# Performance work log

Hardware: AMD Instinct MI355X
Metric: run time of the kernel (lower is better)

## Reference

```python
import jax, jax.numpy as jnp
import numpy as np

B, S, D_MODEL, H = 4, 2048, 1024, 16
DEPTH = D_MODEL // H  # 64


def setup_inputs() -> dict:
    key = jax.random.key(0)
    ks = jax.random.split(key, 12)
    inp = {
        "v": jax.random.normal(ks[0], (B, S, D_MODEL), jnp.float32),
        "k": jax.random.normal(ks[1], (B, S, D_MODEL), jnp.float32),
        "q": jax.random.normal(ks[2], (B, S, D_MODEL), jnp.float32),
        "mask": jnp.zeros((B, 1, 1, S), jnp.int32),  # unused by the layer
        # Dense(d_model) params (glorot-ish scale)
        "wq": jax.random.normal(ks[3], (D_MODEL, D_MODEL), jnp.float32) / np.sqrt(D_MODEL),
        "bq": jnp.zeros((D_MODEL,), jnp.float32),
        "wk": jax.random.normal(ks[4], (D_MODEL, D_MODEL), jnp.float32) / np.sqrt(D_MODEL),
        "bk": jnp.zeros((D_MODEL,), jnp.float32),
        "wv": jax.random.normal(ks[5], (D_MODEL, D_MODEL), jnp.float32) / np.sqrt(D_MODEL),
        "bv": jnp.zeros((D_MODEL,), jnp.float32),
        # global attention weights: [max_seq_len, 1], stddev=0.1
        "gqw": 0.1 * jax.random.normal(ks[6], (S, 1), jnp.float32),
        "gkw": 0.1 * jax.random.normal(ks[7], (S, 1), jnp.float32),
        "wo": jax.random.normal(ks[8], (D_MODEL, D_MODEL), jnp.float32) / np.sqrt(D_MODEL),
        "bo": jnp.zeros((D_MODEL,), jnp.float32),
    }
    return inp


def _split_heads(x):
    # [B, S, D] -> [B, H, S, depth]
    Bc = x.shape[0]
    return x.reshape(Bc, -1, H, DEPTH).transpose(0, 2, 1, 3)


def reference(v, k, q, mask, wq, bq, wk, bk, wv, bv, gqw, gkw, wo, bo):
    # QKV projections
    qh = _split_heads(q @ wq + bq)  # [B, H, S, depth]
    kh = _split_heads(k @ wk + bk)
    vh = _split_heads(v @ wv + bv)
    # Fastformer additive attention: mul -> seq-sum -> mul -> seq-sum -> mul -> add
    qh = qh * gqw                          # gqw [S,1] broadcasts over [B,H,S,depth]
    gq = jnp.sum(qh, axis=2, keepdims=True)  # global query [B,H,1,depth]
    kh = kh * gq * gkw
    gk = jnp.sum(kh, axis=2, keepdims=True)  # global key [B,H,1,depth]
    out = vh * gk + qh                       # [B,H,S,depth]
    # merge heads and output projection
    out = out.transpose(0, 2, 1, 3).reshape(out.shape[0], -1, D_MODEL)
    return out @ wo + bo
```

## Files before the change

### kernel.cpp

```cpp
#include <hip/hip_runtime.h>

#define DM 1024
#define BATCH 4
#define SEQ 2048
#define M_TOT (BATCH*SEQ)

typedef unsigned short ushort_t;
typedef __bf16 bf16x8 __attribute__((ext_vector_type(8)));
typedef float f32x4 __attribute__((ext_vector_type(4)));
typedef unsigned short u16x8 __attribute__((ext_vector_type(8)));

__device__ __forceinline__ ushort_t f2bf(float f) {
  unsigned u = __builtin_bit_cast(unsigned, f);
  u = (u + 0x7fffu + ((u >> 16) & 1u)) >> 16;
  return (ushort_t)u;
}
__device__ __forceinline__ float bf2f(ushort_t h) {
  unsigned u = ((unsigned)h) << 16;
  return __builtin_bit_cast(float, u);
}

#define GLL(gp, lp)                                                            \
  __builtin_amdgcn_global_load_lds(                                            \
      (const __attribute__((address_space(1))) unsigned int*)(const void*)(gp),\
      (__attribute__((address_space(3))) unsigned int*)(void*)(lp), 16, 0, 0)

__global__ void k_reduce(const float* __restrict__ q, const float* __restrict__ k,
                         const float* __restrict__ v,
                         const float* __restrict__ gqw, const float* __restrict__ gkw,
                         float* __restrict__ qr, float* __restrict__ kr,
                         float* __restrict__ G,
                         ushort_t* __restrict__ qb, ushort_t* __restrict__ vb) {
  const int b = blockIdx.x, dch = blockIdx.y, sch = blockIdx.z;
  const int d = dch * 256 + threadIdx.x;
  const int s0 = sch * (SEQ / 16);
  const size_t base = ((size_t)b * SEQ + s0) * DM + d;
  const float* qp = q + base;
  const float* kp = k + base;
  const float* vp = v + base;
  float aq = 0.f, ak = 0.f;
  for (int i = 0; i < SEQ / 16; ++i) {
    const float qv = qp[(size_t)i * DM];
    aq += gqw[s0 + i] * qv;
    ak += gkw[s0 + i] * kp[(size_t)i * DM];
    qb[base + (size_t)i * DM] = f2bf(qv);
    vb[base + (size_t)i * DM] = f2bf(vp[(size_t)i * DM]);
  }
  atomicAdd(&qr[b * DM + d], aq);
  atomicAdd(&kr[b * DM + d], ak);
  if (b == 0 && dch == 0 && threadIdx.x < SEQ / 16) {
    atomicAdd(&G[0], gqw[s0 + threadIdx.x]);
    atomicAdd(&G[1], gkw[s0 + threadIdx.x]);
  }
}

__global__ void k_gpart(const float* __restrict__ wq, const float* __restrict__ wk,
                        const float* __restrict__ qr, const float* __restrict__ kr,
                        float* __restrict__ qacc, float* __restrict__ kacc) {
  const int d = blockIdx.x * 256 + threadIdx.x;
  const int k0 = blockIdx.y * 32;
  __shared__ float sq[4][32], sk[4][32];
  if (threadIdx.x < 128) {
    const int b = threadIdx.x >> 5, kk = threadIdx.x & 31;
    sq[b][kk] = qr[b * DM + k0 + kk];
    sk[b][kk] = kr[b * DM + k0 + kk];
  }
  __syncthreads();
  float aq[4] = {0.f, 0.f, 0.f, 0.f}, ak[4] = {0.f, 0.f, 0.f, 0.f};
#pragma unroll 8
  for (int kk = 0; kk < 32; ++kk) {
    const float wqv = wq[(size_t)(k0 + kk) * DM + d];
    const float wkv = wk[(size_t)(k0 + kk) * DM + d];
#pragma unroll
    for (int b = 0; b < 4; ++b) {
      aq[b] += sq[b][kk] * wqv;
      ak[b] += sk[b][kk] * wkv;
    }
  }
#pragma unroll
  for (int b = 0; b < 4; ++b) {
    atomicAdd(&qacc[b * DM + d], aq[b]);
    atomicAdd(&kacc[b * DM + d], ak[b]);
  }
}

__global__ void k_gfin(const float* __restrict__ qacc, const float* __restrict__ kacc,
                       const float* __restrict__ bq, const float* __restrict__ bk,
                       const float* __restrict__ G, float* __restrict__ gk) {
  const int i = blockIdx.x * 256 + threadIdx.x;
  const int d = i & (DM - 1);
  const float gqv = qacc[i] + bq[d] * G[0];
  const float gkr = kacc[i] + bk[d] * G[1];
  gk[i] = gqv * gkr;
}

__global__ void k_trans(const float* __restrict__ w0, const float* __restrict__ w1,
                        const float* __restrict__ w2,
                        ushort_t* __restrict__ t0, ushort_t* __restrict__ t1,
                        ushort_t* __restrict__ t2) {
  __shared__ float ls[32][33];
  const float* W = blockIdx.z == 0 ? w0 : (blockIdx.z == 1 ? w1 : w2);
  ushort_t* T = blockIdx.z == 0 ? t0 : (blockIdx.z == 1 ? t1 : t2);
  const int bi = blockIdx.x, bj = blockIdx.y;
#pragma unroll
  for (int p = 0; p < 4; ++p) {
    int e = threadIdx.x + p * 256;
    int r = e >> 5, c = e & 31;
    ls[r][c] = W[(size_t)(bi * 32 + r) * DM + bj * 32 + c];
  }
  __syncthreads();
#pragma unroll
  for (int p = 0; p < 4; ++p) {
    int e = threadIdx.x + p * 256;
    int r = e >> 5, c = e & 31;
    T[(size_t)(bj * 32 + r) * DM + bi * 32 + c] = f2bf(ls[c][r]);
  }
}

__global__ void k_mid(const ushort_t* __restrict__ Vp, const ushort_t* __restrict__ Qs,
                      const float* __restrict__ gk, ushort_t* __restrict__ mid) {
  const size_t i = (size_t)blockIdx.x * 256 + threadIdx.x;
  const int col8 = (int)(i & 127) * 8;
  const int b = (int)(i >> 18);
  u16x8 vv = *(const u16x8*)(Vp + i * 8);
  u16x8 qq = *(const u16x8*)(Qs + i * 8);
  const float4 g0 = *(const float4*)(gk + b * DM + col8);
  const float4 g1 = *(const float4*)(gk + b * DM + col8 + 4);
  float g[8] = {g0.x, g0.y, g0.z, g0.w, g1.x, g1.y, g1.z, g1.w};
  u16x8 o;
#pragma unroll
  for (int j = 0; j < 8; ++j) o[j] = f2bf(bf2f(vv[j]) * g[j] + bf2f(qq[j]));
  *(u16x8*)(mid + i * 8) = o;
}

template <int MODE>
__global__ void k_gemm_db(const ushort_t* __restrict__ A0, const ushort_t* __restrict__ B0,
                          const float* __restrict__ bias0,
                          const ushort_t* __restrict__ A1, const ushort_t* __restrict__ B1,
                          const float* __restrict__ bias1,
                          const float* __restrict__ rs,
                          void* __restrict__ Out0V, void* __restrict__ Out1V) {
  __shared__ __align__(16) ushort_t lsA[3][128 * 32];
  __shared__ __align__(16) ushort_t lsB[3][128 * 32];
  const int z = (MODE == 0) ? blockIdx.z : 0;
  const ushort_t* A  = z ? A1 : A0;
  const ushort_t* Bt = z ? B1 : B0;
  const float* bias  = z ? bias1 : bias0;

  const int tid = threadIdx.x;
  const int w = tid >> 6, lane = tid & 63;
  const int m0 = blockIdx.x * 128, n0 = blockIdx.y * 128;
  const int wr = w >> 1, wc = w & 1;

  const int c0 = w * 2, c1 = c0 + 1;
  const int e0 = c0 * 64 + lane, e1 = c1 * 64 + lane;
  const ushort_t* gA0 = A + (size_t)(m0 + (e0 >> 2)) * DM + (e0 & 3) * 8;
  const ushort_t* gA1 = A + (size_t)(m0 + (e1 >> 2)) * DM + (e1 & 3) * 8;
  const ushort_t* gB0 = Bt + (size_t)(n0 + (e0 >> 2)) * DM + (e0 & 3) * 8;
  const ushort_t* gB1 = Bt + (size_t)(n0 + (e1 >> 2)) * DM + (e1 & 3) * 8;

  int aoff[4], boff[4];
#pragma unroll
  for (int i = 0; i < 4; ++i) {
    aoff[i] = (wr * 64 + i * 16 + (lane & 15)) * 32 + (lane >> 4) * 8;
    boff[i] = (wc * 64 + i * 16 + (lane & 15)) * 32 + (lane >> 4) * 8;
  }

  f32x4 acc[4][4];
#pragma unroll
  for (int i = 0; i < 4; ++i)
#pragma unroll
    for (int j = 0; j < 4; ++j) acc[i][j] = (f32x4){0.f, 0.f, 0.f, 0.f};

  auto STAGE = [&](int buf) {
    GLL(gA0, &lsA[buf][c0 * 512]);
    GLL(gA1, &lsA[buf][c1 * 512]);
    GLL(gB0, &lsB[buf][c0 * 512]);
    GLL(gB1, &lsB[buf][c1 * 512]);
    gA0 += 32; gA1 += 32; gB0 += 32; gB1 += 32;
  };

  STAGE(0);
  STAGE(1);
  int cur = 0, nxt = 2;
#pragma unroll 1
  for (int t = 0; t < 32; ++t) {
    if (t < 31) { asm volatile("s_waitcnt vmcnt(4)" ::: "memory"); }
    else        { asm volatile("s_waitcnt vmcnt(0)" ::: "memory"); }
    __builtin_amdgcn_s_barrier();
    if (t + 2 < 32) {
      STAGE(nxt);
      nxt = (nxt == 2) ? 0 : nxt + 1;
    }
    bf16x8 av[4], bv[4];
#pragma unroll
    for (int i = 0; i < 4; ++i) av[i] = *(const bf16x8*)(&lsA[cur][aoff[i]]);
#pragma unroll
    for (int j = 0; j < 4; ++j) bv[j] = *(const bf16x8*)(&lsB[cur][boff[j]]);
#pragma unroll
    for (int i = 0; i < 4; ++i)
#pragma unroll
      for (int j = 0; j < 4; ++j)
        acc[i][j] = __builtin_amdgcn_mfma_f32_16x16x32_bf16(av[i], bv[j], acc[i][j], 0, 0, 0);
    cur = (cur == 2) ? 0 : cur + 1;
  }

  const int lr = (lane >> 4) * 4, lc = lane & 15;
  const int rbase = m0 + wr * 64, cbase = n0 + wc * 64;
  if constexpr (MODE == 0) {
    if (z == 0) {
      ushort_t* Out = (ushort_t*)Out0V;
#pragma unroll
      for (int j = 0; j < 4; ++j) {
        const int col = cbase + j * 16 + lc;
        const float bs = bias[col];
#pragma unroll
        for (int i = 0; i < 4; ++i)
#pragma unroll
          for (int t = 0; t < 4; ++t) {
            const int row = rbase + i * 16 + lr + t;
            Out[(size_t)row * DM + col] = f2bf((acc[i][j][t] + bs) * rs[row & (SEQ - 1)]);
          }
      }
    } else {
      ushort_t* Out = (ushort_t*)Out1V;
#pragma unroll
      for (int j = 0; j < 4; ++j) {
        const int col = cbase + j * 16 + lc;
        const float bs = bias[col];
#pragma unroll
        for (int i = 0; i < 4; ++i)
#pragma unroll
          for (int t = 0; t < 4; ++t) {
            const int row = rbase + i * 16 + lr + t;
            Out[(size_t)row * DM + col] = f2bf(acc[i][j][t] + bs);
          }
      }
    }
  } else {
    float* Out = (float*)Out0V;
#pragma unroll
    for (int j = 0; j < 4; ++j) {
      const int col = cbase + j * 16 + lc;
      const float bs = bias[col];
#pragma unroll
      for (int i = 0; i < 4; ++i)
#pragma unroll
        for (int t = 0; t < 4; ++t) {
          const int row = rbase + i * 16 + lr + t;
          Out[(size_t)row * DM + col] = acc[i][j][t] + bs;
        }
    }
  }
}

extern "C" void kernel_launch(void* const* d_in, const int* in_sizes, int n_in,
                              void* d_out, int out_size, void* d_ws, size_t ws_size,
                              hipStream_t stream) {
  const float* v   = (const float*)d_in[0];
  const float* k   = (const float*)d_in[1];
  const float* q   = (const float*)d_in[2];
  const float* wq  = (const float*)d_in[4];
  const float* bq  = (const float*)d_in[5];
  const float* wk  = (const float*)d_in[6];
  const float* bk  = (const float*)d_in[7];
  const float* wv  = (const float*)d_in[8];
  const float* bv  = (const float*)d_in[9];
  const float* gqw = (const float*)d_in[10];
  const float* gkw = (const float*)d_in[11];
  const float* wo  = (const float*)d_in[12];
  const float* bo  = (const float*)d_in[13];
  float* out = (float*)d_out;
  float* wsf = (float*)d_ws;

  float* qr   = wsf + 0;
  float* kr   = wsf + 4096;
  float* qacc = wsf + 8192;
  float* kacc = wsf + 12288;
  float* G    = wsf + 16384;
  float* gk   = wsf + 16896;
  ushort_t* qb  = (ushort_t*)((char*)d_ws + (1 << 17));
  ushort_t* vb  = qb + (size_t)M_TOT * DM;
  ushort_t* QsB = vb + (size_t)M_TOT * DM;
  ushort_t* wqT = QsB + (size_t)M_TOT * DM;
  ushort_t* wvT = wqT + (size_t)DM * DM;
  ushort_t* woT = wvT + (size_t)DM * DM;
  ushort_t* midB = qb;
  ushort_t* VpB  = (ushort_t*)out;

  hipMemsetAsync(d_ws, 0, (16384 + 2) * sizeof(float), stream);

  k_reduce<<<dim3(BATCH, DM / 256, 16), 256, 0, stream>>>(q, k, v, gqw, gkw, qr, kr, G, qb, vb);

  k_gpart<<<dim3(DM / 256, DM / 32), 256, 0, stream>>>(wq, wk, qr, kr, qacc, kacc);
  k_gfin<<<(BATCH * DM) / 256, 256, 0, stream>>>(qacc, kacc, bq, bk, G, gk);

  k_trans<<<dim3(32, 32, 3), 256, 0, stream>>>(wq, wv, wo, wqT, wvT, woT);

  k_gemm_db<0><<<dim3(M_TOT / 128, DM / 128, 2), 256, 0, stream>>>(
      qb, wqT, bq, vb, wvT, bv, gqw, QsB, VpB);

  k_mid<<<(M_TOT * (DM / 8)) / 256, 256, 0, stream>>>(VpB, QsB, gk, midB);

  k_gemm_db<1><<<dim3(M_TOT / 128, DM / 128), 256, 0, stream>>>(
      midB, woT, bo, nullptr, nullptr, nullptr, nullptr, out, nullptr);
}
```

Baseline: 143.3 us.

## Fold output projection into Q/V weights and fuse both GEMMs into one

Uses associativity to precompute Wq·Wo and per-batch Wv·diag(gk)·Wo with small 1024^3 GEMMs. The big path then becomes a single K=2048 GEMM over concatenated [gqw·q | v] activations. This removes the separate projection GEMM, the elementwise mid kernel and the bf16 intermediate round-trips. Bias terms are folded into per-column epilogue vectors. The cost is five small weight GEMMs per call and an extra bf16 rounding of the combined weights, which may change accuracy.

```diff
diff --git a/kernel.cpp b/kernel.cpp
--- a/kernel.cpp
+++ b/kernel.cpp
@@ -40,10 +40,11 @@
   const float* vp = v + base;
   float aq = 0.f, ak = 0.f;
   for (int i = 0; i < SEQ / 16; ++i) {
+    const float w = gqw[s0 + i];
     const float qv = qp[(size_t)i * DM];
-    aq += gqw[s0 + i] * qv;
+    aq += w * qv;
     ak += gkw[s0 + i] * kp[(size_t)i * DM];
-    qb[base + (size_t)i * DM] = f2bf(qv);
+    qb[base + (size_t)i * DM] = f2bf(w * qv);
     vb[base + (size_t)i * DM] = f2bf(vp[(size_t)i * DM]);
   }
   atomicAdd(&qr[b * DM + d], aq);
@@ -94,13 +95,18 @@
   gk[i] = gqv * gkr;
 }
 
-__global__ void k_trans(const float* __restrict__ w0, const float* __restrict__ w1,
-                        const float* __restrict__ w2,
-                        ushort_t* __restrict__ t0, ushort_t* __restrict__ t1,
-                        ushort_t* __restrict__ t2) {
+__global__ void k_conv(const float* __restrict__ x, ushort_t* __restrict__ y) {
+  size_t i = (size_t)blockIdx.x * 256 + threadIdx.x;
+  const float4* p = (const float4*)x + i * 2;
+  float4 a = p[0], b = p[1];
+  u16x8 o;
+  o[0] = f2bf(a.x); o[1] = f2bf(a.y); o[2] = f2bf(a.z); o[3] = f2bf(a.w);
+  o[4] = f2bf(b.x); o[5] = f2bf(b.y); o[6] = f2bf(b.z); o[7] = f2bf(b.w);
+  *(u16x8*)(y + i * 8) = o;
+}
+
+__global__ void k_trans(const float* __restrict__ W, ushort_t* __restrict__ T) {
   __shared__ float ls[32][33];
-  const float* W = blockIdx.z == 0 ? w0 : (blockIdx.z == 1 ? w1 : w2);
-  ushort_t* T = blockIdx.z == 0 ? t0 : (blockIdx.z == 1 ? t1 : t2);
   const int bi = blockIdx.x, bj = blockIdx.y;
 #pragma unroll
   for (int p = 0; p < 4; ++p) {
@@ -117,41 +123,54 @@
   }
 }
 
-__global__ void k_mid(const ushort_t* __restrict__ Vp, const ushort_t* __restrict__ Qs,
-                      const float* __restrict__ gk, ushort_t* __restrict__ mid) {
+__global__ void k_wog(const ushort_t* __restrict__ woT, const float* __restrict__ gk,
+                      ushort_t* __restrict__ wogT) {
   const size_t i = (size_t)blockIdx.x * 256 + threadIdx.x;
-  const int col8 = (int)(i & 127) * 8;
-  const int b = (int)(i >> 18);
-  u16x8 vv = *(const u16x8*)(Vp + i * 8);
-  u16x8 qq = *(const u16x8*)(Qs + i * 8);
-  const float4 g0 = *(const float4*)(gk + b * DM + col8);
-  const float4 g1 = *(const float4*)(gk + b * DM + col8 + 4);
+  const size_t c = i * 8;
+  const int j0 = (int)(c & (DM - 1));
+  const int b = (int)(c >> 20);
+  u16x8 wv = *(const u16x8*)(woT + (c & ((1u << 20) - 1)));
+  const float4 g0 = *(const float4*)(gk + b * DM + j0);
+  const float4 g1 = *(const float4*)(gk + b * DM + j0 + 4);
   float g[8] = {g0.x, g0.y, g0.z, g0.w, g1.x, g1.y, g1.z, g1.w};
   u16x8 o;
 #pragma unroll
-  for (int j = 0; j < 8; ++j) o[j] = f2bf(bf2f(vv[j]) * g[j] + bf2f(qq[j]));
-  *(u16x8*)(mid + i * 8) = o;
-}
-
-template <int MODE>
-__global__ void k_gemm_db(const ushort_t* __restrict__ A0, const ushort_t* __restrict__ B0,
-                          const float* __restrict__ bias0,
-                          const ushort_t* __restrict__ A1, const ushort_t* __restrict__ B1,
-                          const float* __restrict__ bias1,
-                          const float* __restrict__ rs,
-                          void* __restrict__ Out0V, void* __restrict__ Out1V) {
+  for (int j = 0; j < 8; ++j) o[j] = f2bf(bf2f(wv[j]) * g[j]);
+  *(u16x8*)(wogT + i * 8) = o;
+}
+
+__global__ void k_bias(const float* __restrict__ wo, const float* __restrict__ bq,
+                       const float* __restrict__ bv, const float* __restrict__ gk,
+                       float* __restrict__ qbias, float* __restrict__ vbias) {
+  const int n = blockIdx.x * 256 + threadIdx.x;
+  const int k0 = blockIdx.y * 32;
+  float aq = 0.f, av[4] = {0.f, 0.f, 0.f, 0.f};
+  for (int kk = 0; kk < 32; ++kk) {
+    const float w = wo[(size_t)(k0 + kk) * DM + n];
+    aq += bq[k0 + kk] * w;
+    const float bw = bv[k0 + kk] * w;
+#pragma unroll
+    for (int b = 0; b < 4; ++b) av[b] += bw * gk[b * DM + k0 + kk];
+  }
+  atomicAdd(&qbias[n], aq);
+#pragma unroll
+  for (int b = 0; b < 4; ++b) atomicAdd(&vbias[b * DM + n], av[b]);
+}
+
+__global__ void k_small(const ushort_t* __restrict__ woT, const ushort_t* __restrict__ wogT,
+                        const ushort_t* __restrict__ wqB, const ushort_t* __restrict__ wvB,
+                        ushort_t* __restrict__ WqoT, ushort_t* __restrict__ WvbT) {
   __shared__ __align__(16) ushort_t lsA[3][128 * 32];
   __shared__ __align__(16) ushort_t lsB[3][128 * 32];
-  const int z = (MODE == 0) ? blockIdx.z : 0;
-  const ushort_t* A  = z ? A1 : A0;
-  const ushort_t* Bt = z ? B1 : B0;
-  const float* bias  = z ? bias1 : bias0;
+  const int z = blockIdx.z;
+  const ushort_t* A  = z == 0 ? woT : wogT + (size_t)(z - 1) * (DM * DM);
+  const ushort_t* Bt = z == 0 ? wqB : wvB;
+  ushort_t* Out      = z == 0 ? WqoT : WvbT + (size_t)(z - 1) * (DM * DM);
 
   const int tid = threadIdx.x;
   const int w = tid >> 6, lane = tid & 63;
   const int m0 = blockIdx.x * 128, n0 = blockIdx.y * 128;
   const int wr = w >> 1, wc = w & 1;
-
   const int c0 = w * 2, c1 = c0 + 1;
   const int e0 = c0 * 64 + lane, e1 = c1 * 64 + lane;
   const ushort_t* gA0 = A + (size_t)(m0 + (e0 >> 2)) * DM + (e0 & 3) * 8;
@@ -172,16 +191,16 @@
 #pragma unroll
     for (int j = 0; j < 4; ++j) acc[i][j] = (f32x4){0.f, 0.f, 0.f, 0.f};
 
-  auto STAGE = [&](int buf) {
-    GLL(gA0, &lsA[buf][c0 * 512]);
-    GLL(gA1, &lsA[buf][c1 * 512]);
-    GLL(gB0, &lsB[buf][c0 * 512]);
-    GLL(gB1, &lsB[buf][c1 * 512]);
-    gA0 += 32; gA1 += 32; gB0 += 32; gB1 += 32;
+  auto STAGE = [&](int tt, int buf) {
+    const int o = tt * 32;
+    GLL(gA0 + o, &lsA[buf][c0 * 512]);
+    GLL(gA1 + o, &lsA[buf][c1 * 512]);
+    GLL(gB0 + o, &lsB[buf][c0 * 512]);
+    GLL(gB1 + o, &lsB[buf][c1 * 512]);
   };
 
-  STAGE(0);
-  STAGE(1);
+  STAGE(0, 0);
+  STAGE(1, 1);
   int cur = 0, nxt = 2;
 #pragma unroll 1
   for (int t = 0; t < 32; ++t) {
@@ -189,7 +208,7 @@
     else        { asm volatile("s_waitcnt vmcnt(0)" ::: "memory"); }
     __builtin_amdgcn_s_barrier();
     if (t + 2 < 32) {
-      STAGE(nxt);
+      STAGE(t + 2, nxt);
       nxt = (nxt == 2) ? 0 : nxt + 1;
     }
     bf16x8 av[4], bv[4];
@@ -207,50 +226,113 @@
 
   const int lr = (lane >> 4) * 4, lc = lane & 15;
   const int rbase = m0 + wr * 64, cbase = n0 + wc * 64;
-  if constexpr (MODE == 0) {
-    if (z == 0) {
-      ushort_t* Out = (ushort_t*)Out0V;
-#pragma unroll
-      for (int j = 0; j < 4; ++j) {
-        const int col = cbase + j * 16 + lc;
-        const float bs = bias[col];
-#pragma unroll
-        for (int i = 0; i < 4; ++i)
-#pragma unroll
-          for (int t = 0; t < 4; ++t) {
-            const int row = rbase + i * 16 + lr + t;
-            Out[(size_t)row * DM + col] = f2bf((acc[i][j][t] + bs) * rs[row & (SEQ - 1)]);
-          }
+#pragma unroll
+  for (int j = 0; j < 4; ++j) {
+    const int col = cbase + j * 16 + lc;
+#pragma unroll
+    for (int i = 0; i < 4; ++i)
+#pragma unroll
+      for (int t = 0; t < 4; ++t) {
+        const int row = rbase + i * 16 + lr + t;
+        Out[(size_t)row * DM + col] = f2bf(acc[i][j][t]);
       }
+  }
+}
+
+__global__ void k_big(const ushort_t* __restrict__ qb, const ushort_t* __restrict__ vb,
+                      const ushort_t* __restrict__ WqoT, const ushort_t* __restrict__ WvbT,
+                      const float* __restrict__ gqw, const float* __restrict__ qbias,
+                      const float* __restrict__ vbias, const float* __restrict__ bo,
+                      float* __restrict__ Out) {
+  __shared__ __align__(16) ushort_t lsA[3][128 * 32];
+  __shared__ __align__(16) ushort_t lsB[3][128 * 32];
+  const int tid = threadIdx.x;
+  const int w = tid >> 6, lane = tid & 63;
+  const int m0 = blockIdx.x * 128, n0 = blockIdx.y * 128;
+  const int b = m0 >> 11;
+  const int wr = w >> 1, wc = w & 1;
+  const int c0 = w * 2, c1 = c0 + 1;
+  const int e0 = c0 * 64 + lane, e1 = c1 * 64 + lane;
+  const size_t offA0 = (size_t)(m0 + (e0 >> 2)) * DM + (e0 & 3) * 8;
+  const size_t offA1 = (size_t)(m0 + (e1 >> 2)) * DM + (e1 & 3) * 8;
+  const size_t offB0 = (size_t)(n0 + (e0 >> 2)) * DM + (e0 & 3) * 8;
+  const size_t offB1 = (size_t)(n0 + (e1 >> 2)) * DM + (e1 & 3) * 8;
+  const ushort_t* gAq0 = qb + offA0;
+  const ushort_t* gAq1 = qb + offA1;
+  const ushort_t* gAv0 = vb + offA0;
+  const ushort_t* gAv1 = vb + offA1;
+  const ushort_t* gBq0 = WqoT + offB0;
+  const ushort_t* gBq1 = WqoT + offB1;
+  const ushort_t* gBv0 = WvbT + (size_t)b * (DM * DM) + offB0;
+  const ushort_t* gBv1 = WvbT + (size_t)b * (DM * DM) + offB1;
+
+  int aoff[4], boff[4];
+#pragma unroll
+  for (int i = 0; i < 4; ++i) {
+    aoff[i] = (wr * 64 + i * 16 + (lane & 15)) * 32 + (lane >> 4) * 8;
+    boff[i] = (wc * 64 + i * 16 + (lane & 15)) * 32 + (lane >> 4) * 8;
+  }
+
+  f32x4 acc[4][4];
+#pragma unroll
+  for (int i = 0; i < 4; ++i)
+#pragma unroll
+    for (int j = 0; j < 4; ++j) acc[i][j] = (f32x4){0.f, 0.f, 0.f, 0.f};
+
+  auto STAGE = [&](int tt, int buf) {
+    const ushort_t *a0, *a1, *b0, *b1;
+    if (tt < 32) {
+      const int o = tt * 32;
+      a0 = gAq0 + o; a1 = gAq1 + o; b0 = gBq0 + o; b1 = gBq1 + o;
     } else {
-      ushort_t* Out = (ushort_t*)Out1V;
-#pragma unroll
-      for (int j = 0; j < 4; ++j) {
-        const int col = cbase + j * 16 + lc;
-        const float bs = bias[col];
-#pragma unroll
-        for (int i = 0; i < 4; ++i)
-#pragma unroll
-          for (int t = 0; t < 4; ++t) {
-            const int row = rbase + i * 16 + lr + t;
-            Out[(size_t)row * DM + col] = f2bf(acc[i][j][t] + bs);
-          }
+      const int o = (tt - 32) * 32;
+      a0 = gAv0 + o; a1 = gAv1 + o; b0 = gBv0 + o; b1 = gBv1 + o;
+    }
+    GLL(a0, &lsA[buf][c0 * 512]);
+    GLL(a1, &lsA[buf][c1 * 512]);
+    GLL(b0, &lsB[buf][c0 * 512]);
+    GLL(b1, &lsB[buf][c1 * 512]);
+  };
+
+  STAGE(0, 0);
+  STAGE(1, 1);
+  int cur = 0, nxt = 2;
+#pragma unroll 1
+  for (int t = 0; t < 64; ++t) {
+    if (t < 63) { asm volatile("s_waitcnt vmcnt(4)" ::: "memory"); }
+    else        { asm volatile("s_waitcnt vmcnt(0)" ::: "memory"); }
+    __builtin_amdgcn_s_barrier();
+    if (t + 2 < 64) {
+      STAGE(t + 2, nxt);
+      nxt = (nxt == 2) ? 0 : nxt + 1;
+    }
+    bf16x8 av[4], bv[4];
+#pragma unroll
+    for (int i = 0; i < 4; ++i) av[i] = *(const bf16x8*)(&lsA[cur][aoff[i]]);
+#pragma unroll
+    for (int j = 0; j < 4; ++j) bv[j] = *(const bf16x8*)(&lsB[cur][boff[j]]);
+#pragma unroll
+    for (int i = 0; i < 4; ++i)
+#pragma unroll
+      for (int j = 0; j < 4; ++j)
+        acc[i][j] = __builtin_amdgcn_mfma_f32_16x16x32_bf16(av[i], bv[j], acc[i][j], 0, 0, 0);
+    cur = (cur == 2) ? 0 : cur + 1;
+  }
+
+  const int lr = (lane >> 4) * 4, lc = lane & 15;
+  const int rbase = m0 + wr * 64, cbase = n0 + wc * 64;
+#pragma unroll
+  for (int j = 0; j < 4; ++j) {
+    const int col = cbase + j * 16 + lc;
+    const float qbn = qbias[col];
+    const float cb = vbias[b * DM + col] + bo[col];
+#pragma unroll
+    for (int i = 0; i < 4; ++i)
+#pragma unroll
+      for (int t = 0; t < 4; ++t) {
+        const int row = rbase + i * 16 + lr + t;
+        Out[(size_t)row * DM + col] = acc[i][j][t] + gqw[row & (SEQ - 1)] * qbn + cb;
       }
-    }
-  } else {
-    float* Out = (float*)Out0V;
-#pragma unroll
-    for (int j = 0; j < 4; ++j) {
-      const int col = cbase + j * 16 + lc;
-      const float bs = bias[col];
-#pragma unroll
-      for (int i = 0; i < 4; ++i)
-#pragma unroll
-        for (int t = 0; t < 4; ++t) {
-          const int row = rbase + i * 16 + lr + t;
-          Out[(size_t)row * DM + col] = acc[i][j][t] + bs;
-        }
-    }
   }
 }
 
@@ -273,35 +355,40 @@
   float* out = (float*)d_out;
   float* wsf = (float*)d_ws;
 
-  float* qr   = wsf + 0;
-  float* kr   = wsf + 4096;
-  float* qacc = wsf + 8192;
-  float* kacc = wsf + 12288;
-  float* G    = wsf + 16384;
-  float* gk   = wsf + 16896;
-  ushort_t* qb  = (ushort_t*)((char*)d_ws + (1 << 17));
-  ushort_t* vb  = qb + (size_t)M_TOT * DM;
-  ushort_t* QsB = vb + (size_t)M_TOT * DM;
-  ushort_t* wqT = QsB + (size_t)M_TOT * DM;
-  ushort_t* wvT = wqT + (size_t)DM * DM;
-  ushort_t* woT = wvT + (size_t)DM * DM;
-  ushort_t* midB = qb;
-  ushort_t* VpB  = (ushort_t*)out;
-
-  hipMemsetAsync(d_ws, 0, (16384 + 2) * sizeof(float), stream);
+  float* qr    = wsf + 0;
+  float* kr    = wsf + 4096;
+  float* qacc  = wsf + 8192;
+  float* kacc  = wsf + 12288;
+  float* G     = wsf + 16384;
+  float* qbias = wsf + 16640;
+  float* vbias = wsf + 17664;
+  float* gk    = wsf + 21760;
+  ushort_t* b16  = (ushort_t*)((char*)d_ws + (1 << 17));
+  ushort_t* qb   = b16;
+  ushort_t* vb   = qb + (size_t)M_TOT * DM;
+  ushort_t* wqB  = vb + (size_t)M_TOT * DM;
+  ushort_t* wvB  = wqB + (size_t)DM * DM;
+  ushort_t* woT  = wvB + (size_t)DM * DM;
+  ushort_t* WqoT = woT + (size_t)DM * DM;
+  ushort_t* WvbT = WqoT + (size_t)DM * DM;
+  ushort_t* wogT = (ushort_t*)out;
+
+  hipMemsetAsync(d_ws, 0, 21760 * sizeof(float), stream);
+
+  k_conv<<<(DM * DM / 8) / 256, 256, 0, stream>>>(wq, wqB);
+  k_conv<<<(DM * DM / 8) / 256, 256, 0, stream>>>(wv, wvB);
+  k_trans<<<dim3(32, 32), 256, 0, stream>>>(wo, woT);
 
   k_reduce<<<dim3(BATCH, DM / 256, 16), 256, 0, stream>>>(q, k, v, gqw, gkw, qr, kr, G, qb, vb);
 
   k_gpart<<<dim3(DM / 256, DM / 32), 256, 0, stream>>>(wq, wk, qr, kr, qacc, kacc);
   k_gfin<<<(BATCH * DM) / 256, 256, 0, stream>>>(qacc, kacc, bq, bk, G, gk);
 
-  k_trans<<<dim3(32, 32, 3), 256, 0, stream>>>(wq, wv, wo, wqT, wvT, woT);
-
-  k_gemm_db<0><<<dim3(M_TOT / 128, DM / 128, 2), 256, 0, stream>>>(
-      qb, wqT, bq, vb, wvT, bv, gqw, QsB, VpB);
-
-  k_mid<<<(M_TOT * (DM / 8)) / 256, 256, 0, stream>>>(VpB, QsB, gk, midB);
-
-  k_gemm_db<1><<<dim3(M_TOT / 128, DM / 128), 256, 0, stream>>>(
-      midB, woT, bo, nullptr, nullptr, nullptr, nullptr, out, nullptr);
-}
+  k_wog<<<(BATCH * DM * DM / 8) / 256, 256, 0, stream>>>(woT, gk, wogT);
+  k_bias<<<dim3(DM / 256, DM / 32), 256, 0, stream>>>(wo, bq, bv, gk, qbias, vbias);
+
+  k_small<<<dim3(8, 8, 5), 256, 0, stream>>>(woT, wogT, wqB, wvB, WqoT, WvbT);
+
+  k_big<<<dim3(M_TOT / 128, DM / 128), 256, 0, stream>>>(
+      qb, vb, WqoT, WvbT, gqw, qbias, vbias, bo, out);
+}
```

After: 143.3 us. Within noise of the previous version (-0.0%).
